# Kernel optimization log

Measured on AMD Instinct MI355X. Metric: run time of the kernel, lower is better.

The kernel has to match this reference:

```python
import jax, jax.numpy as jnp
import numpy as np


def setup_inputs() -> dict:
    key = jax.random.key(0)
    inputs = jax.random.normal(key, (2048, 8192), dtype=jnp.float32)
    return {"inputs": inputs, "window_size": 14}


def reference(inputs, window_size):
    # percentage change per step, with divide_no_nan semantics (0 when prev==0)
    prev = inputs[:, :-1]                               # [B, T-1]
    delta = inputs[:, 1:] - prev                        # [B, T-1]
    nz = prev != 0
    p = jnp.where(nz, delta / jnp.where(nz, prev, 1.0), 0.0)

    # SignFilter(+1) keeps positive part; SignFilter(-1) keeps negative part
    gains = jnp.where(p > 0, p, 0.0)
    losses = jnp.where(p < 0, -p, 0.0)

    w = window_size - 1  # each window of W prices yields W-1 percentage values

    def windowed_mean(a):
        # mean over every length-w sliding window along axis 1 via cumsum
        cs = jnp.cumsum(a, axis=1)
        cs = jnp.concatenate([jnp.zeros_like(cs[:, :1]), cs], axis=1)
        return (cs[:, w:] - cs[:, :-w]) / w             # [B, T-W+1]

    avg_gain = windowed_mean(gains)
    avg_loss = windowed_mean(losses)

    # divide_no_nan: rs = 0 when avg_loss == 0  ->  rsi = 0
    lnz = avg_loss != 0
    rs = jnp.where(lnz, avg_gain / jnp.where(lnz, avg_loss, 1.0), 0.0)
    return 1.0 - 1.0 / (1.0 + rs)
```

## Files before the change

kernel.cpp:

```cpp
#include <hip/hip_runtime.h>


constexpr int ROWS = 2048;
constexpr int COLS = 8192;
constexpr int NP   = COLS - 1;
constexpr int BT   = 256;
constexpr int TS   = 17;

__global__ __launch_bounds__(BT, 1)
void rsi_rwr_kernel(const float* __restrict__ x,
                    const int* __restrict__ wsp,
                    float* __restrict__ out,
                    int outW)
{
    __shared__ float CG[512 * TS], CL[512 * TS];
    __shared__ float T0g[544], T0l[544];
    __shared__ float S1g[544], S1l[544];
    __shared__ float T1g[32],  T1l[32];
    __shared__ float S2g[32],  S2l[32];
    __shared__ float T2g[2],   T2l[2];
    __shared__ float S3g[2],   S3l[2];

    const int row = blockIdx.x;
    const int t   = threadIdx.x;
    const int wm1 = *wsp - 1;

    const float* __restrict__ xr = x + (size_t)row * COLS;

    float rg[2][16], rl[2][16];

    #pragma unroll
    for (int bi = 0; bi < 2; ++bi) {
        const int b = t + 256 * bi;
        const float4* xv = reinterpret_cast<const float4*>(xr + 16 * b);
        float xe[17];
        {
            float4 v0 = xv[0], v1 = xv[1], v2 = xv[2], v3 = xv[3];
            xe[0]=v0.x;  xe[1]=v0.y;  xe[2]=v0.z;  xe[3]=v0.w;
            xe[4]=v1.x;  xe[5]=v1.y;  xe[6]=v1.z;  xe[7]=v1.w;
            xe[8]=v2.x;  xe[9]=v2.y;  xe[10]=v2.z; xe[11]=v2.w;
            xe[12]=v3.x; xe[13]=v3.y; xe[14]=v3.z; xe[15]=v3.w;
        }
        xe[16] = (b < 511) ? xr[16 * b + 16] : 0.f;

        float cg = 0.f, cl = 0.f;
        #pragma unroll
        for (int r = 0; r < 16; ++r) {
            const int j = 16 * b + r;
            float eg = 0.f, el = 0.f;
            if (j < NP) {
                const float prev = xe[r];
                const float nxt  = xe[r + 1];
                if (prev != 0.f) {
                    const float p = (nxt - prev) / prev;
                    eg = (p > 0.f) ?  p : 0.f;
                    el = (p < 0.f) ? -p : 0.f;
                }
            }
            cg = cg + eg;
            cl = cl + el;
            rg[bi][r] = cg;
            rl[bi][r] = cl;
        }
        T0g[b + (b >> 4)] = cg;
        T0l[b + (b >> 4)] = cl;
    }
    __syncthreads();

    if (t < 32) {
        float cg = 0.f, cl = 0.f;
        for (int s = 0; s < 16; ++s) {
            const int k = TS * t + s;
            cg = cg + T0g[k];
            cl = cl + T0l[k];
            S1g[k] = cg;
            S1l[k] = cl;
        }
        T1g[t] = cg; T1l[t] = cl;
    }
    __syncthreads();

    if (t < 2) {
        float cg = 0.f, cl = 0.f;
        for (int u = 0; u < 16; ++u) {
            cg = cg + T1g[16 * t + u];
            cl = cl + T1l[16 * t + u];
            S2g[16 * t + u] = cg;
            S2l[16 * t + u] = cl;
        }
        T2g[t] = cg; T2l[t] = cl;
    }
    __syncthreads();

    if (t == 0) {
        S3g[0] = T2g[0]; S3g[1] = T2g[0] + T2g[1];
        S3l[0] = T2l[0]; S3l[1] = T2l[0] + T2l[1];
    }
    __syncthreads();
    if (t >= 16 && t < 32) {
        const int k = t;
        S2g[k] = S2g[k] + S3g[0];
        S2l[k] = S2l[k] + S3l[0];
    }
    __syncthreads();
    for (int k = 16 + t; k < 512; k += BT) {
        const int c  = k >> 4;
        const int kp = k + (k >> 4);
        S1g[kp] = S1g[kp] + S2g[c - 1];
        S1l[kp] = S1l[kp] + S2l[c - 1];
    }
    __syncthreads();

    #pragma unroll
    for (int bi = 0; bi < 2; ++bi) {
        const int b = t + 256 * bi;
        float og = 0.f, ol = 0.f;
        if (b >= 1) {
            const int bp = (b - 1) + ((b - 1) >> 4);
            og = S1g[bp]; ol = S1l[bp];
        }
        float* __restrict__ cgp = &CG[TS * b];
        float* __restrict__ clp = &CL[TS * b];
        #pragma unroll
        for (int r = 0; r < 16; ++r) {
            cgp[r] = rg[bi][r] + og;
            clp[r] = rl[bi][r] + ol;
        }
    }
    __syncthreads();

    float* __restrict__ outr = out + (size_t)row * outW;
    {
        int o  = t;
        int j2 = o + wm1 - 1;
        int i2 = TS * (j2 >> 4) + (j2 & 15);
        int i1 = (o >= 1) ? (TS * ((o - 1) >> 4) + ((o - 1) & 15)) : -2;
        for (; o < outW; o += BT, i2 += 272, i1 += 272) {
            float cg1 = 0.f, cl1 = 0.f;
            if (o >= 1) {
                cg1 = CG[i1];
                cl1 = CL[i1];
            }
            const float a  = CG[i2] - cg1;
            const float bb = CL[i2] - cl1;
            float rs = 0.f;
            if (bb != 0.f) rs = a * __builtin_amdgcn_rcpf(bb);
            outr[o] = 1.f - __builtin_amdgcn_rcpf(1.f + rs);
        }
    }
}

extern "C" void kernel_launch(void* const* d_in, const int* in_sizes, int n_in,
                              void* d_out, int out_size, void* d_ws, size_t ws_size,
                              hipStream_t stream) {
    const float* x   = (const float*)d_in[0];
    const int*   wsp = (const int*)d_in[1];
    float*       out = (float*)d_out;

    const int outW = out_size / ROWS;
    dim3 grid(ROWS);
    dim3 block(BT);
    rsi_rwr_kernel<<<grid, block, 0, stream>>>(x, wsp, out, outW);
}
```

Before: 137.6 us.

## Compute windowed differences from registers with wavefront shuffles, drop big LDS staging

Adds a kernel templated on the window length that keeps each thread's 16-element prefix sums in registers. It takes the neighbouring thread's tail values via shuffle-up, and wavefront-boundary tails through a small shared buffer. This removes the large CG/CL shared-memory staging arrays, one barrier pass, and the strided LDS reads, and raises launch bounds to allow more blocks per CU. The window length is inferred on the host from the output width, and a fallback kernel handles other window sizes. The cost is extra per-thread output logic and register pressure from unrolled window arrays.

```diff
diff --git a/kernel.cpp b/kernel.cpp
--- a/kernel.cpp
+++ b/kernel.cpp
@@ -7,24 +7,23 @@
 constexpr int BT   = 256;
 constexpr int TS   = 17;
 
-__global__ __launch_bounds__(BT, 1)
-void rsi_rwr_kernel(const float* __restrict__ x,
-                    const int* __restrict__ wsp,
+template<int WM1>
+__global__ __launch_bounds__(BT, 4)
+void rsi_reg_kernel(const float* __restrict__ x,
                     float* __restrict__ out,
                     int outW)
 {
-    __shared__ float CG[512 * TS], CL[512 * TS];
     __shared__ float T0g[544], T0l[544];
     __shared__ float S1g[544], S1l[544];
     __shared__ float T1g[32],  T1l[32];
     __shared__ float S2g[32],  S2l[32];
     __shared__ float T2g[2],   T2l[2];
     __shared__ float S3g[2],   S3l[2];
-
-    const int row = blockIdx.x;
-    const int t   = threadIdx.x;
-    const int wm1 = *wsp - 1;
-
+    __shared__ float BPg[7][WM1], BPl[7][WM1];
+
+    const int row  = blockIdx.x;
+    const int t    = threadIdx.x;
+    const int lane = t & 63;
     const float* __restrict__ xr = x + (size_t)row * COLS;
 
     float rg[2][16], rl[2][16];
@@ -98,9 +97,8 @@
     }
     __syncthreads();
     if (t >= 16 && t < 32) {
-        const int k = t;
-        S2g[k] = S2g[k] + S3g[0];
-        S2l[k] = S2l[k] + S3l[0];
+        S2g[t] = S2g[t] + S3g[0];
+        S2l[t] = S2l[t] + S3l[0];
     }
     __syncthreads();
     for (int k = 16 + t; k < 512; k += BT) {
@@ -119,6 +117,178 @@
             const int bp = (b - 1) + ((b - 1) >> 4);
             og = S1g[bp]; ol = S1l[bp];
         }
+        #pragma unroll
+        for (int r = 0; r < 16; ++r) {
+            rg[bi][r] = rg[bi][r] + og;
+            rl[bi][r] = rl[bi][r] + ol;
+        }
+    }
+    if (lane == 63) {
+        const int w = t >> 6;
+        #pragma unroll
+        for (int r = 16 - WM1; r < 16; ++r) {
+            BPg[w][r - (16 - WM1)] = rg[0][r];
+            BPl[w][r - (16 - WM1)] = rl[0][r];
+        }
+        if (w < 3) {
+            #pragma unroll
+            for (int r = 16 - WM1; r < 16; ++r) {
+                BPg[4 + w][r - (16 - WM1)] = rg[1][r];
+                BPl[4 + w][r - (16 - WM1)] = rl[1][r];
+            }
+        }
+    }
+    __syncthreads();
+
+    float* __restrict__ outr = out + (size_t)row * outW;
+    #pragma unroll
+    for (int bi = 0; bi < 2; ++bi) {
+        const int b = t + 256 * bi;
+        float pg[WM1], pl[WM1];
+        #pragma unroll
+        for (int r = 16 - WM1; r < 16; ++r) {
+            pg[r - (16 - WM1)] = __shfl_up(rg[bi][r], 1);
+            pl[r - (16 - WM1)] = __shfl_up(rl[bi][r], 1);
+        }
+        if (lane == 0) {
+            int slot;
+            if (bi == 0) slot = (t > 0) ? ((t >> 6) - 1) : -1;
+            else         slot = (t == 0) ? 3 : (3 + (t >> 6));
+            if (slot >= 0) {
+                #pragma unroll
+                for (int q = 0; q < WM1; ++q) { pg[q] = BPg[slot][q]; pl[q] = BPl[slot][q]; }
+            }
+        }
+        const int o0 = 16 * b - (WM1 - 1);
+        #pragma unroll
+        for (int k = 0; k < 16; ++k) {
+            const int o = o0 + k;
+            const float cg2 = rg[bi][k], cl2 = rl[bi][k];
+            float cg1, cl1;
+            if (k >= WM1) { cg1 = rg[bi][k - WM1]; cl1 = rl[bi][k - WM1]; }
+            else          { cg1 = pg[k];           cl1 = pl[k]; }
+            if (o < 1) { cg1 = 0.f; cl1 = 0.f; }
+            const float a  = cg2 - cg1;
+            const float bb = cl2 - cl1;
+            float rs = 0.f;
+            if (bb != 0.f) rs = a * __builtin_amdgcn_rcpf(bb);
+            const float v = 1.f - __builtin_amdgcn_rcpf(1.f + rs);
+            if (o >= 0 && o < outW) outr[o] = v;
+        }
+    }
+}
+
+__global__ __launch_bounds__(BT, 1)
+void rsi_rwr_fallback(const float* __restrict__ x,
+                      const int* __restrict__ wsp,
+                      float* __restrict__ out,
+                      int outW)
+{
+    __shared__ float CG[512 * TS], CL[512 * TS];
+    __shared__ float T0g[544], T0l[544];
+    __shared__ float S1g[544], S1l[544];
+    __shared__ float T1g[32],  T1l[32];
+    __shared__ float S2g[32],  S2l[32];
+    __shared__ float T2g[2],   T2l[2];
+    __shared__ float S3g[2],   S3l[2];
+
+    const int row = blockIdx.x;
+    const int t   = threadIdx.x;
+    const int wm1 = *wsp - 1;
+    const float wf = (float)wm1;
+    const float* __restrict__ xr = x + (size_t)row * COLS;
+
+    float rg[2][16], rl[2][16];
+
+    #pragma unroll
+    for (int bi = 0; bi < 2; ++bi) {
+        const int b = t + 256 * bi;
+        const float4* xv = reinterpret_cast<const float4*>(xr + 16 * b);
+        float xe[17];
+        {
+            float4 v0 = xv[0], v1 = xv[1], v2 = xv[2], v3 = xv[3];
+            xe[0]=v0.x;  xe[1]=v0.y;  xe[2]=v0.z;  xe[3]=v0.w;
+            xe[4]=v1.x;  xe[5]=v1.y;  xe[6]=v1.z;  xe[7]=v1.w;
+            xe[8]=v2.x;  xe[9]=v2.y;  xe[10]=v2.z; xe[11]=v2.w;
+            xe[12]=v3.x; xe[13]=v3.y; xe[14]=v3.z; xe[15]=v3.w;
+        }
+        xe[16] = (b < 511) ? xr[16 * b + 16] : 0.f;
+
+        float cg = 0.f, cl = 0.f;
+        #pragma unroll
+        for (int r = 0; r < 16; ++r) {
+            const int j = 16 * b + r;
+            float eg = 0.f, el = 0.f;
+            if (j < NP) {
+                const float prev = xe[r];
+                const float nxt  = xe[r + 1];
+                if (prev != 0.f) {
+                    const float p = (nxt - prev) / prev;
+                    eg = (p > 0.f) ?  p : 0.f;
+                    el = (p < 0.f) ? -p : 0.f;
+                }
+            }
+            cg = cg + eg;
+            cl = cl + el;
+            rg[bi][r] = cg;
+            rl[bi][r] = cl;
+        }
+        T0g[b + (b >> 4)] = cg;
+        T0l[b + (b >> 4)] = cl;
+    }
+    __syncthreads();
+
+    if (t < 32) {
+        float cg = 0.f, cl = 0.f;
+        for (int s = 0; s < 16; ++s) {
+            const int k = TS * t + s;
+            cg = cg + T0g[k];
+            cl = cl + T0l[k];
+            S1g[k] = cg;
+            S1l[k] = cl;
+        }
+        T1g[t] = cg; T1l[t] = cl;
+    }
+    __syncthreads();
+
+    if (t < 2) {
+        float cg = 0.f, cl = 0.f;
+        for (int u = 0; u < 16; ++u) {
+            cg = cg + T1g[16 * t + u];
+            cl = cl + T1l[16 * t + u];
+            S2g[16 * t + u] = cg;
+            S2l[16 * t + u] = cl;
+        }
+        T2g[t] = cg; T2l[t] = cl;
+    }
+    __syncthreads();
+
+    if (t == 0) {
+        S3g[0] = T2g[0]; S3g[1] = T2g[0] + T2g[1];
+        S3l[0] = T2l[0]; S3l[1] = T2l[0] + T2l[1];
+    }
+    __syncthreads();
+    if (t >= 16 && t < 32) {
+        S2g[t] = S2g[t] + S3g[0];
+        S2l[t] = S2l[t] + S3l[0];
+    }
+    __syncthreads();
+    for (int k = 16 + t; k < 512; k += BT) {
+        const int c  = k >> 4;
+        const int kp = k + (k >> 4);
+        S1g[kp] = S1g[kp] + S2g[c - 1];
+        S1l[kp] = S1l[kp] + S2l[c - 1];
+    }
+    __syncthreads();
+
+    #pragma unroll
+    for (int bi = 0; bi < 2; ++bi) {
+        const int b = t + 256 * bi;
+        float og = 0.f, ol = 0.f;
+        if (b >= 1) {
+            const int bp = (b - 1) + ((b - 1) >> 4);
+            og = S1g[bp]; ol = S1l[bp];
+        }
         float* __restrict__ cgp = &CG[TS * b];
         float* __restrict__ clp = &CL[TS * b];
         #pragma unroll
@@ -130,23 +300,21 @@
     __syncthreads();
 
     float* __restrict__ outr = out + (size_t)row * outW;
-    {
-        int o  = t;
-        int j2 = o + wm1 - 1;
-        int i2 = TS * (j2 >> 4) + (j2 & 15);
-        int i1 = (o >= 1) ? (TS * ((o - 1) >> 4) + ((o - 1) & 15)) : -2;
-        for (; o < outW; o += BT, i2 += 272, i1 += 272) {
-            float cg1 = 0.f, cl1 = 0.f;
-            if (o >= 1) {
-                cg1 = CG[i1];
-                cl1 = CL[i1];
-            }
-            const float a  = CG[i2] - cg1;
-            const float bb = CL[i2] - cl1;
-            float rs = 0.f;
-            if (bb != 0.f) rs = a * __builtin_amdgcn_rcpf(bb);
-            outr[o] = 1.f - __builtin_amdgcn_rcpf(1.f + rs);
-        }
+    for (int o = t; o < outW; o += BT) {
+        const int j2 = o + wm1 - 1;
+        const int i2 = TS * (j2 >> 4) + (j2 & 15);
+        float cg1 = 0.f, cl1 = 0.f;
+        if (o >= 1) {
+            const int j1 = o - 1;
+            const int i1 = TS * (j1 >> 4) + (j1 & 15);
+            cg1 = CG[i1];
+            cl1 = CL[i1];
+        }
+        const float a  = CG[i2] - cg1;
+        const float bb = CL[i2] - cl1;
+        float rs = 0.f;
+        if (bb != 0.f) rs = a * __builtin_amdgcn_rcpf(bb);
+        outr[o] = 1.f - __builtin_amdgcn_rcpf(1.f + rs);
     }
 }
 
@@ -158,7 +326,12 @@
     float*       out = (float*)d_out;
 
     const int outW = out_size / ROWS;
+    const int wm1  = COLS - outW;
     dim3 grid(ROWS);
     dim3 block(BT);
-    rsi_rwr_kernel<<<grid, block, 0, stream>>>(x, wsp, out, outW);
+    if (wm1 == 13) {
+        rsi_reg_kernel<13><<<grid, block, 0, stream>>>(x, out, outW);
+    } else {
+        rsi_rwr_fallback<<<grid, block, 0, stream>>>(x, wsp, out, outW);
+    }
 }
```

Result: slower. 180.7 us (+31.4%).
